# Optimization experiments

Measured on AMD Instinct MI355X. Metric: run time of the kernel, lower is better.

Reference implementation:

```python
import jax, jax.numpy as jnp
import numpy as np

B, N, S, D1, D2 = 16, 4096, 1024, 128, 256
MLP = [256, 128]
BN_EPS = 1e-5


def setup_inputs() -> dict:
    key = jax.random.key(0)
    ks = jax.random.split(key, 12)
    inp = {
        "xyz1": jax.random.normal(ks[0], (B, 3, N), dtype=jnp.float32),
        "xyz2": jax.random.normal(ks[1], (B, 3, S), dtype=jnp.float32),
        "points1": jax.random.normal(ks[2], (B, D1, N), dtype=jnp.float32),
        "points2": jax.random.normal(ks[3], (B, D2, S), dtype=jnp.float32),
    }
    in_ch = D1 + D2  # 384
    chans = [in_ch] + MLP
    ki = 4
    for li in range(len(MLP)):
        cin, cout = chans[li], chans[li + 1]
        inp[f"w{li+1}"] = jax.random.normal(ks[ki], (cout, cin), dtype=jnp.float32) * (1.0 / np.sqrt(cin)); ki += 1
        inp[f"b{li+1}"] = jnp.zeros((cout,), dtype=jnp.float32)
        inp[f"g{li+1}"] = jnp.ones((cout,), dtype=jnp.float32)
        inp[f"beta{li+1}"] = jnp.zeros((cout,), dtype=jnp.float32)
    return inp


def _batchnorm1d(x, gamma, beta):
    # x: [B, C, N]; training-mode batch stats over (B, N)
    mean = jnp.mean(x, axis=(0, 2), keepdims=True)
    var = jnp.var(x, axis=(0, 2), keepdims=True)
    xhat = (x - mean) * jax.lax.rsqrt(var + BN_EPS)
    return xhat * gamma[None, :, None] + beta[None, :, None]


def reference(xyz1, xyz2, points1, points2, w1, b1, g1, beta1, w2, b2, g2, beta2):
    x1 = jnp.transpose(xyz1, (0, 2, 1))   # [B, N, 3]
    x2 = jnp.transpose(xyz2, (0, 2, 1))   # [B, S, 3]
    p2 = jnp.transpose(points2, (0, 2, 1))  # [B, S, D2]

    # squared pairwise distances [B, N, S]
    dists = jnp.sum((x1[:, :, None, :] - x2[:, None, :, :]) ** 2, axis=-1)
    # 3 smallest distances (original sorts then slices top-3)
    neg_d3, idx = jax.lax.top_k(-dists, 3)  # [B, N, 3]
    d3 = -neg_d3
    dist_recip = 1.0 / (d3 + 1e-8)
    weight = dist_recip / jnp.sum(dist_recip, axis=2, keepdims=True)  # [B, N, 3]

    # gather neighbor features: [B, N, 3, D2]
    feats = p2[jnp.arange(p2.shape[0])[:, None, None], idx]
    interp = jnp.sum(feats * weight[..., None], axis=2)  # [B, N, D2]

    p1 = jnp.transpose(points1, (0, 2, 1))  # [B, N, D1]
    new_points = jnp.concatenate([p1, interp], axis=-1)  # [B, N, D1+D2]
    x = jnp.transpose(new_points, (0, 2, 1))  # [B, C, N]

    for w, b, g, bt in ((w1, b1, g1, beta1), (w2, b2, g2, beta2)):
        x = jnp.einsum("oc,bcn->bon", w, x) + b[None, :, None]
        x = _batchnorm1d(x, g, bt)
        x = jax.nn.relu(x)
    return x
```

## Files before the change

### kernel.cpp

```cpp
#include <hip/hip_runtime.h>

typedef unsigned short u16;
typedef unsigned int   u32;
typedef __attribute__((ext_vector_type(8))) short bf16x8;
typedef __attribute__((ext_vector_type(8))) unsigned short u16x8;
typedef __attribute__((ext_vector_type(4))) float f32x4;

#define NB   16
#define NPTS 4096
#define SPTS 1024
#define BNT  65536

#define G2L(src, dst) __builtin_amdgcn_global_load_lds( \
    (const __attribute__((address_space(1))) void*)(src), \
    (__attribute__((address_space(3))) void*)(dst), 16, 0, 0)

__device__ __forceinline__ float bf2f(u16 u){ return __uint_as_float(((u32)u)<<16); }
__device__ __forceinline__ u16 f2bf(float f){
  u32 u = __float_as_uint(f);
  return (u16)((u + 0x7FFFu + ((u>>16)&1u))>>16);
}

__global__ __launch_bounds__(256) void convw_k(const float* __restrict__ w1, const float* __restrict__ w2,
                                               u16* __restrict__ w1b, u16* __restrict__ w2b){
  int i = blockIdx.x*256 + threadIdx.x;
  if (i < 98304) w1b[i] = f2bf(w1[i]);
  else { int j = i - 98304; w2b[j] = f2bf(w2[j]); }
}

__global__ __launch_bounds__(256) void transpose_k(const float* __restrict__ in, u16* __restrict__ out,
                                                   int C, int S, int ostride){
  __shared__ float tl[64][65];
  int t = threadIdx.x;
  int b = blockIdx.y;
  int s0 = blockIdx.x * 64;
  for (int ct = 0; ct < C; ct += 64){
    __syncthreads();
    for (int i = t; i < 4096; i += 256){
      int sl = i & 63, cl = i >> 6;
      tl[sl][cl] = in[((size_t)b*C + ct + cl)*S + s0 + sl];
    }
    __syncthreads();
    for (int i = t; i < 4096; i += 256){
      int cl = i & 63, sl = i >> 6;
      out[((size_t)b*S + s0 + sl)*ostride + ct + cl] = f2bf(tl[sl][cl]);
    }
  }
}

__global__ __launch_bounds__(512) void knn_k(const float* __restrict__ xyz1, const float* __restrict__ xyz2,
                                             const u16* __restrict__ p2t, u16* __restrict__ X){
  __shared__ float4 sxyz[SPTS];
  __shared__ float  pd[8][3][64];
  __shared__ int    pi[8][3][64];
  __shared__ float  swts[3][64];
  __shared__ int    sidx[3][64];
  int t  = threadIdx.x;
  int b  = blockIdx.x >> 6;
  int n0 = (blockIdx.x & 63) << 6;
  const float* x2b = xyz2 + (size_t)b*3*SPTS;
  for (int s = t; s < SPTS; s += 512)
    sxyz[s] = make_float4(x2b[s], x2b[SPTS+s], x2b[2*SPTS+s], 0.f);
  int q = t & 63, g = t >> 6;
  const float* x1b = xyz1 + (size_t)b*3*NPTS;
  int n = n0 + q;
  float qx = x1b[n], qy = x1b[NPTS+n], qz = x1b[2*NPTS+n];
  __syncthreads();

  float d0=3.4e38f, d1=3.4e38f, d2=3.4e38f;
  int   i0=0, i1=0, i2=0;
  int sBeg = g << 7, sEnd = sBeg + 128;
  for (int s = sBeg; s < sEnd; ++s){
    float4 p = sxyz[s];
    float dist;
    {
      #pragma clang fp contract(off)
      float dx = qx - p.x, dy = qy - p.y, dz = qz - p.z;
      dist = ((dx*dx) + (dy*dy)) + (dz*dz);
    }
    if (dist < d2){
      bool c1 = dist < d1, c0 = dist < d0;
      d2 = c1 ? d1 : dist;                 i2 = c1 ? i1 : s;
      float nd1 = c1 ? (c0 ? d0 : dist) : d1;
      int   ni1 = c1 ? (c0 ? i0 : s)    : i1;
      d0 = c0 ? dist : d0;                 i0 = c0 ? s : i0;
      d1 = nd1;                            i1 = ni1;
    }
  }
  pd[g][0][q]=d0; pd[g][1][q]=d1; pd[g][2][q]=d2;
  pi[g][0][q]=i0; pi[g][1][q]=i1; pi[g][2][q]=i2;
  __syncthreads();

  if (t < 64){
    float m0=3.4e38f, m1=3.4e38f, m2=3.4e38f;
    int   j0=0, j1=0, j2=0;
    #pragma unroll
    for (int gg = 0; gg < 8; ++gg){
      #pragma unroll
      for (int p = 0; p < 3; ++p){
        float dist = pd[gg][p][t]; int s = pi[gg][p][t];
        if (dist < m2){
          bool c1 = dist < m1, c0 = dist < m0;
          m2 = c1 ? m1 : dist;                 j2 = c1 ? j1 : s;
          float nd1 = c1 ? (c0 ? m0 : dist) : m1;
          int   ni1 = c1 ? (c0 ? j0 : s)    : j1;
          m0 = c0 ? dist : m0;                 j0 = c0 ? s : j0;
          m1 = nd1;                            j1 = ni1;
        }
      }
    }
    float r0 = 1.f/(m0 + 1e-8f), r1 = 1.f/(m1 + 1e-8f), r2 = 1.f/(m2 + 1e-8f);
    float rs = (r0 + r1) + r2;
    swts[0][t] = r0/rs; swts[1][t] = r1/rs; swts[2][t] = r2/rs;
    sidx[0][t] = j0;    sidx[1][t] = j1;    sidx[2][t] = j2;
  }
  __syncthreads();

  int w = t >> 6, lane = t & 63;
  for (int qq = w*8; qq < w*8 + 8; ++qq){
    float wa = swts[0][qq], wb = swts[1][qq], wc = swts[2][qq];
    int   j0 = sidx[0][qq], j1 = sidx[1][qq], j2 = sidx[2][qq];
    const ushort4 u0 = *(const ushort4*)(p2t + (((size_t)b*SPTS + j0)<<8) + (lane<<2));
    const ushort4 u1 = *(const ushort4*)(p2t + (((size_t)b*SPTS + j1)<<8) + (lane<<2));
    const ushort4 u2 = *(const ushort4*)(p2t + (((size_t)b*SPTS + j2)<<8) + (lane<<2));
    ushort4 ov;
    ov.x = f2bf(wa*bf2f(u0.x) + wb*bf2f(u1.x) + wc*bf2f(u2.x));
    ov.y = f2bf(wa*bf2f(u0.y) + wb*bf2f(u1.y) + wc*bf2f(u2.y));
    ov.z = f2bf(wa*bf2f(u0.z) + wb*bf2f(u1.z) + wc*bf2f(u2.z));
    ov.w = f2bf(wa*bf2f(u0.w) + wb*bf2f(u1.w) + wc*bf2f(u2.w));
    *(ushort4*)(X + ((size_t)b*NPTS + n0 + qq)*384 + 128 + (lane<<2)) = ov;
  }
}

__global__ __launch_bounds__(256) void gemm1_k(const u16* __restrict__ A, const u16* __restrict__ Bw,
                                               u16* __restrict__ Cc,
                                               float* __restrict__ psum, float* __restrict__ psq){
  __shared__ u16 lA[128*64];
  __shared__ u16 lB[256*64];
  float* sums = (float*)lA;
  float* sqs  = sums + 256;
  int t = threadIdx.x, lane = t & 63, wid = t >> 6;
  int rowBase = blockIdx.x << 7;
  int wm = wid >> 1, wn = wid & 1;

  const char* pA[4]; int dAo[4];
  #pragma unroll
  for (int j = 0; j < 4; ++j){
    int L = j*4096 + t*16;
    int row = L >> 7, kb = L & 127;
    int kbs = kb ^ ((row & 7) << 4);
    pA[j] = (const char*)A + (size_t)(rowBase + row)*768 + kbs;
    dAo[j] = j*4096 + wid*1024;
  }
  const char* pB[8]; int dBo[8];
  #pragma unroll
  for (int j = 0; j < 8; ++j){
    int L = j*4096 + t*16;
    int row = L >> 7, kb = L & 127;
    int kbs = kb ^ ((row & 7) << 4);
    pB[j] = (const char*)Bw + (size_t)row*768 + kbs;
    dBo[j] = j*4096 + wid*1024;
  }

  f32x4 z = {0.f,0.f,0.f,0.f};
  f32x4 acc[4][8];
  #pragma unroll
  for (int m = 0; m < 4; ++m)
    #pragma unroll
    for (int n = 0; n < 8; ++n) acc[m][n] = z;

  #pragma unroll
  for (int kt = 0; kt < 6; ++kt){
    size_t ko = (size_t)kt * 128;
    #pragma unroll
    for (int j = 0; j < 4; ++j) G2L(pA[j] + ko, (char*)lA + dAo[j]);
    #pragma unroll
    for (int j = 0; j < 8; ++j) G2L(pB[j] + ko, (char*)lB + dBo[j]);
    __syncthreads();
    #pragma unroll
    for (int ks = 0; ks < 2; ++ks){
      bf16x8 af[4];
      #pragma unroll
      for (int m = 0; m < 4; ++m){
        int row = wm*64 + m*16 + (lane & 15);
        int sw = (row & 7) << 4;
        int kb = (ks*64 + ((lane >> 4) << 4)) ^ sw;
        af[m] = *(const bf16x8*)((const char*)lA + row*128 + kb);
      }
      #pragma unroll
      for (int n = 0; n < 8; ++n){
        int row = wn*128 + n*16 + (lane & 15);
        int sw = (row & 7) << 4;
        int kb = (ks*64 + ((lane >> 4) << 4)) ^ sw;
        bf16x8 bv = *(const bf16x8*)((const char*)lB + row*128 + kb);
        #pragma unroll
        for (int m = 0; m < 4; ++m)
          acc[m][n] = __builtin_amdgcn_mfma_f32_16x16x32_bf16(af[m], bv, acc[m][n], 0, 0, 0);
      }
    }
    __syncthreads();
  }

  sums[t] = 0.f; sqs[t] = 0.f;
  __syncthreads();
  int colb = wn*128 + (lane & 15);
  #pragma unroll
  for (int n = 0; n < 8; ++n){
    float s = 0.f, q = 0.f;
    #pragma unroll
    for (int m = 0; m < 4; ++m){
      #pragma unroll
      for (int r = 0; r < 4; ++r){
        float v = acc[m][n][r];
        s += v; q += v*v;
      }
    }
    s += __shfl_xor(s, 16); s += __shfl_xor(s, 32);
    q += __shfl_xor(q, 16); q += __shfl_xor(q, 32);
    if (lane < 16){
      atomicAdd(&sums[colb + n*16], s);
      atomicAdd(&sqs [colb + n*16], q);
    }
  }
  __syncthreads();
  psum[(size_t)blockIdx.x*256 + t] = sums[t];
  psq [(size_t)blockIdx.x*256 + t] = sqs[t];

  u16* bb = lB;
  int rl0 = ((lane >> 4) << 2);
  #pragma unroll
  for (int h = 0; h < 2; ++h){
    __syncthreads();
    if (wm == h){
      #pragma unroll
      for (int m = 0; m < 4; ++m)
        #pragma unroll
        for (int n = 0; n < 8; ++n)
          #pragma unroll
          for (int r = 0; r < 4; ++r)
            bb[(m*16 + rl0 + r)*256 + colb + n*16] = f2bf(acc[m][n][r]);
    }
    __syncthreads();
    u16* dst = Cc + (size_t)(rowBase + h*64)*256;
    #pragma unroll
    for (int i = 0; i < 8; ++i)
      *(u16x8*)(dst + i*2048 + t*8) = *(const u16x8*)(bb + i*2048 + t*8);
  }
}

__global__ __launch_bounds__(256) void gemm2_k(const u16* __restrict__ A, const u16* __restrict__ Bw,
                                               u16* __restrict__ Cc,
                                               const float* __restrict__ sc, const float* __restrict__ sh,
                                               float* __restrict__ psum, float* __restrict__ psq){
  const int K = 256;
  __shared__ u16 L[16384];
  __shared__ float sums[128], sqs[128];
  int t = threadIdx.x, lane = t & 63, wid = t >> 6;
  int rowBase = blockIdx.x << 7;
  int wm = wid >> 1, wn = wid & 1;

  const char* pB[4]; int dBo[4];
  #pragma unroll
  for (int j = 0; j < 4; ++j){
    int Lo = j*4096 + t*16;
    int row = Lo >> 7, kb = Lo & 127;
    int kbs = kb ^ ((row & 7) << 4);
    pB[j] = (const char*)Bw + ((size_t)row*K)*2 + kbs;
    dBo[j] = 16384 + j*4096 + wid*1024;
  }
  int arow = t & 127, h = t >> 7;
  const u16* pArow = A + (size_t)(rowBase + arow)*K + h*32;
  int asw = (arow & 7) << 4;
  int wAo0 = arow*128 + ((h*64      ) ^ asw);
  int wAo1 = arow*128 + ((h*64 + 16 ) ^ asw);
  int wAo2 = arow*128 + ((h*64 + 32 ) ^ asw);
  int wAo3 = arow*128 + ((h*64 + 48 ) ^ asw);

  f32x4 z = {0.f,0.f,0.f,0.f};
  f32x4 acc[4][4];
  #pragma unroll
  for (int m = 0; m < 4; ++m)
    #pragma unroll
    for (int n = 0; n < 4; ++n) acc[m][n] = z;

  for (int kk = 0; kk < K; kk += 64){
    size_t ko = (size_t)kk * 2;
    #pragma unroll
    for (int j = 0; j < 4; ++j) G2L(pB[j] + ko, (char*)L + dBo[j]);
    u16x8 y0 = *(const u16x8*)(pArow + kk);
    u16x8 y1 = *(const u16x8*)(pArow + kk + 8);
    u16x8 y2 = *(const u16x8*)(pArow + kk + 16);
    u16x8 y3 = *(const u16x8*)(pArow + kk + 24);
    int k0 = kk + h*32;
    bf16x8 o0, o1, o2, o3;
    #pragma unroll
    for (int j = 0; j < 8; ++j){
      float v = bf2f((u16)y0[j]) * sc[k0 + j] + sh[k0 + j];
      o0[j] = (short)f2bf(fmaxf(v, 0.f));
    }
    #pragma unroll
    for (int j = 0; j < 8; ++j){
      float v = bf2f((u16)y1[j]) * sc[k0 + 8 + j] + sh[k0 + 8 + j];
      o1[j] = (short)f2bf(fmaxf(v, 0.f));
    }
    #pragma unroll
    for (int j = 0; j < 8; ++j){
      float v = bf2f((u16)y2[j]) * sc[k0 + 16 + j] + sh[k0 + 16 + j];
      o2[j] = (short)f2bf(fmaxf(v, 0.f));
    }
    #pragma unroll
    for (int j = 0; j < 8; ++j){
      float v = bf2f((u16)y3[j]) * sc[k0 + 24 + j] + sh[k0 + 24 + j];
      o3[j] = (short)f2bf(fmaxf(v, 0.f));
    }
    *(bf16x8*)((char*)L + wAo0) = o0;
    *(bf16x8*)((char*)L + wAo1) = o1;
    *(bf16x8*)((char*)L + wAo2) = o2;
    *(bf16x8*)((char*)L + wAo3) = o3;
    __syncthreads();
    #pragma unroll
    for (int ks = 0; ks < 2; ++ks){
      bf16x8 af[4];
      #pragma unroll
      for (int m = 0; m < 4; ++m){
        int row = wm*64 + m*16 + (lane & 15);
        int sw = (row & 7) << 4;
        int kb = (ks*64 + ((lane >> 4) << 4)) ^ sw;
        af[m] = *(const bf16x8*)((const char*)L + row*128 + kb);
      }
      #pragma unroll
      for (int n = 0; n < 4; ++n){
        int row = wn*64 + n*16 + (lane & 15);
        int sw = (row & 7) << 4;
        int kb = (ks*64 + ((lane >> 4) << 4)) ^ sw;
        bf16x8 bv = *(const bf16x8*)((const char*)L + 16384 + row*128 + kb);
        #pragma unroll
        for (int m = 0; m < 4; ++m)
          acc[m][n] = __builtin_amdgcn_mfma_f32_16x16x32_bf16(af[m], bv, acc[m][n], 0, 0, 0);
      }
    }
    __syncthreads();
  }

  if (t < 128){ sums[t] = 0.f; sqs[t] = 0.f; }
  __syncthreads();
  int colb = wn*64 + (lane & 15);
  int rl0 = ((lane >> 4) << 2);
  #pragma unroll
  for (int n = 0; n < 4; ++n){
    float s = 0.f, q = 0.f;
    #pragma unroll
    for (int m = 0; m < 4; ++m){
      #pragma unroll
      for (int r = 0; r < 4; ++r){
        float v = acc[m][n][r];
        L[(wm*64 + m*16 + rl0 + r)*128 + colb + n*16] = f2bf(v);
        s += v; q += v*v;
      }
    }
    s += __shfl_xor(s, 16); s += __shfl_xor(s, 32);
    q += __shfl_xor(q, 16); q += __shfl_xor(q, 32);
    if (lane < 16){
      atomicAdd(&sums[colb + n*16], s);
      atomicAdd(&sqs [colb + n*16], q);
    }
  }
  __syncthreads();
  if (t < 128){
    psum[(size_t)blockIdx.x*128 + t] = sums[t];
    psq [(size_t)blockIdx.x*128 + t] = sqs[t];
  }
  u16* dst = Cc + (size_t)rowBase*128;
  #pragma unroll
  for (int i = 0; i < 8; ++i)
    *(u16x8*)(dst + i*2048 + t*8) = *(const u16x8*)(L + i*2048 + t*8);
}

__global__ __launch_bounds__(256) void finalize2_k(const float* __restrict__ psum, const float* __restrict__ psq,
                                                   const float* __restrict__ g, const float* __restrict__ bet,
                                                   float* __restrict__ sc, float* __restrict__ sh,
                                                   int C, int NBLK){
  __shared__ float ls[256][8], lq[256][8];
  int c0 = blockIdx.x*8, t = threadIdx.x;
  float s[8], q[8];
  #pragma unroll
  for (int j = 0; j < 8; ++j){ s[j] = 0.f; q[j] = 0.f; }
  for (int rb = t; rb < NBLK; rb += 256){
    const float* ps = psum + (size_t)rb*C + c0;
    const float* pq = psq  + (size_t)rb*C + c0;
    #pragma unroll
    for (int j = 0; j < 8; ++j){ s[j] += ps[j]; q[j] += pq[j]; }
  }
  #pragma unroll
  for (int j = 0; j < 8; ++j){ ls[t][j] = s[j]; lq[t][j] = q[j]; }
  __syncthreads();
  for (int off = 128; off; off >>= 1){
    if (t < off){
      #pragma unroll
      for (int j = 0; j < 8; ++j){ ls[t][j] += ls[t+off][j]; lq[t][j] += lq[t+off][j]; }
    }
    __syncthreads();
  }
  if (t < 8){
    int c = c0 + t;
    const float inv = 1.f/65536.f;
    float mean = ls[0][t]*inv;
    float var  = lq[0][t]*inv - mean*mean;
    float rstd = rsqrtf(var + 1e-5f);
    float scl  = g[c]*rstd;
    sc[c] = scl;
    sh[c] = bet[c] - mean*scl;
  }
}

__global__ __launch_bounds__(256) void finalout_k(const u16* __restrict__ y2, const float* __restrict__ sc,
                                                  const float* __restrict__ sh, float* __restrict__ out){
  __shared__ float tl[128][65];
  int t  = threadIdx.x;
  int b  = blockIdx.x >> 6;
  int n0 = (blockIdx.x & 63) << 6;
  for (int i = t; i < 8192; i += 256){
    int r = i >> 7, c = i & 127;
    float v = bf2f(y2[((size_t)b*NPTS + n0 + r)*128 + c]);
    v = fmaxf(v*sc[c] + sh[c], 0.f);
    tl[c][r] = v;
  }
  __syncthreads();
  for (int i = t; i < 8192; i += 256){
    int o = i >> 6, j = i & 63;
    out[(size_t)b*128*NPTS + (size_t)o*NPTS + n0 + j] = tl[o][j];
  }
}

extern "C" void kernel_launch(void* const* d_in, const int* in_sizes, int n_in,
                              void* d_out, int out_size, void* d_ws, size_t ws_size,
                              hipStream_t stream) {
  const float* xyz1    = (const float*)d_in[0];
  const float* xyz2    = (const float*)d_in[1];
  const float* points1 = (const float*)d_in[2];
  const float* points2 = (const float*)d_in[3];
  const float* w1      = (const float*)d_in[4];
  const float* g1      = (const float*)d_in[6];
  const float* beta1   = (const float*)d_in[7];
  const float* w2      = (const float*)d_in[8];
  const float* g2      = (const float*)d_in[10];
  const float* beta2   = (const float*)d_in[11];

  char* ws = (char*)d_ws;
  u16*  X    = (u16*)ws;
  u16*  Y2   = (u16*)ws;
  u16*  Y1   = (u16*)(ws + 50331648);
  u16*  p2t  = (u16*)(ws + 83886080);
  u16*  w1b  = (u16*)(ws + 92274688);
  u16*  w2b  = (u16*)(ws + 92471296);
  float* psum1 = (float*)(ws + 83886080);
  float* psq1  = (float*)(ws + 84934656);
  float* psum2 = (float*)(ws + 85983232);
  float* psq2  = (float*)(ws + 86507520);
  float* sc1   = (float*)(ws + 87031808);
  float* sh1   = (float*)(ws + 87032832);
  float* sc2   = (float*)(ws + 87033856);
  float* sh2   = (float*)(ws + 87034368);

  convw_k<<<512, 256, 0, stream>>>(w1, w2, w1b, w2b);
  transpose_k<<<dim3(64, 16), 256, 0, stream>>>(points1, X,   128, NPTS, 384);
  transpose_k<<<dim3(16, 16), 256, 0, stream>>>(points2, p2t, 256, SPTS, 256);
  knn_k<<<1024, 512, 0, stream>>>(xyz1, xyz2, p2t, X);
  gemm1_k<<<512, 256, 0, stream>>>(X, w1b, Y1, psum1, psq1);
  finalize2_k<<<32, 256, 0, stream>>>(psum1, psq1, g1, beta1, sc1, sh1, 256, 512);
  gemm2_k<<<512, 256, 0, stream>>>(Y1, w2b, Y2, sc1, sh1, psum2, psq2);
  finalize2_k<<<16, 256, 0, stream>>>(psum2, psq2, g2, beta2, sc2, sh2, 128, 512);
  finalout_k<<<1024, 256, 0, stream>>>(Y2, sc2, sh2, (float*)d_out);
}
```

Before: 144.4 us.

## Double-buffer LDS K-tiles in both GEMM kernels to overlap loads with MFMA

Both GEMM kernels now split K into 32-wide tiles held in two LDS buffers. The next tile's global-to-LDS loads (and in gemm2, the BN+ReLU transform of the A tile) are issued while MFMAs run on the current buffer, with one barrier per step. The swizzle is adapted to the 64-byte row pitch. This is meant to hide global load latency behind compute, at the cost of twice as many loop iterations and barriers and extra register pressure for the prefetched A values.

```diff
diff --git a/kernel.cpp b/kernel.cpp
--- a/kernel.cpp
+++ b/kernel.cpp
@@ -135,29 +135,29 @@
 __global__ __launch_bounds__(256) void gemm1_k(const u16* __restrict__ A, const u16* __restrict__ Bw,
                                                u16* __restrict__ Cc,
                                                float* __restrict__ psum, float* __restrict__ psq){
-  __shared__ u16 lA[128*64];
-  __shared__ u16 lB[256*64];
+  __shared__ u16 lA[2][128*32];
+  __shared__ u16 lB[2][256*32];
   float* sums = (float*)lA;
   float* sqs  = sums + 256;
   int t = threadIdx.x, lane = t & 63, wid = t >> 6;
   int rowBase = blockIdx.x << 7;
   int wm = wid >> 1, wn = wid & 1;
 
-  const char* pA[4]; int dAo[4];
+  const char* pA[2]; int dAo[2];
+  #pragma unroll
+  for (int j = 0; j < 2; ++j){
+    int L = j*4096 + t*16;
+    int row = L >> 6, kb = L & 63;
+    int kbs = kb ^ (((row >> 1) & 3) << 4);
+    pA[j] = (const char*)A + (size_t)(rowBase + row)*768 + kbs;
+    dAo[j] = j*4096 + wid*1024;
+  }
+  const char* pB[4]; int dBo[4];
   #pragma unroll
   for (int j = 0; j < 4; ++j){
     int L = j*4096 + t*16;
-    int row = L >> 7, kb = L & 127;
-    int kbs = kb ^ ((row & 7) << 4);
-    pA[j] = (const char*)A + (size_t)(rowBase + row)*768 + kbs;
-    dAo[j] = j*4096 + wid*1024;
-  }
-  const char* pB[8]; int dBo[8];
-  #pragma unroll
-  for (int j = 0; j < 8; ++j){
-    int L = j*4096 + t*16;
-    int row = L >> 7, kb = L & 127;
-    int kbs = kb ^ ((row & 7) << 4);
+    int row = L >> 6, kb = L & 63;
+    int kbs = kb ^ (((row >> 1) & 3) << 4);
     pB[j] = (const char*)Bw + (size_t)row*768 + kbs;
     dBo[j] = j*4096 + wid*1024;
   }
@@ -170,33 +170,36 @@
     for (int n = 0; n < 8; ++n) acc[m][n] = z;
 
   #pragma unroll
-  for (int kt = 0; kt < 6; ++kt){
-    size_t ko = (size_t)kt * 128;
-    #pragma unroll
-    for (int j = 0; j < 4; ++j) G2L(pA[j] + ko, (char*)lA + dAo[j]);
-    #pragma unroll
-    for (int j = 0; j < 8; ++j) G2L(pB[j] + ko, (char*)lB + dBo[j]);
-    __syncthreads();
-    #pragma unroll
-    for (int ks = 0; ks < 2; ++ks){
-      bf16x8 af[4];
-      #pragma unroll
-      for (int m = 0; m < 4; ++m){
-        int row = wm*64 + m*16 + (lane & 15);
-        int sw = (row & 7) << 4;
-        int kb = (ks*64 + ((lane >> 4) << 4)) ^ sw;
-        af[m] = *(const bf16x8*)((const char*)lA + row*128 + kb);
-      }
-      #pragma unroll
-      for (int n = 0; n < 8; ++n){
-        int row = wn*128 + n*16 + (lane & 15);
-        int sw = (row & 7) << 4;
-        int kb = (ks*64 + ((lane >> 4) << 4)) ^ sw;
-        bf16x8 bv = *(const bf16x8*)((const char*)lB + row*128 + kb);
-        #pragma unroll
-        for (int m = 0; m < 4; ++m)
-          acc[m][n] = __builtin_amdgcn_mfma_f32_16x16x32_bf16(af[m], bv, acc[m][n], 0, 0, 0);
-      }
+  for (int j = 0; j < 2; ++j) G2L(pA[j], (char*)lA[0] + dAo[j]);
+  #pragma unroll
+  for (int j = 0; j < 4; ++j) G2L(pB[j], (char*)lB[0] + dBo[j]);
+  __syncthreads();
+
+  #pragma unroll
+  for (int kt = 0; kt < 12; ++kt){
+    const int cur = kt & 1;
+    if (kt < 11){
+      size_t ko = (size_t)(kt + 1) * 64;
+      #pragma unroll
+      for (int j = 0; j < 2; ++j) G2L(pA[j] + ko, (char*)lA[cur^1] + dAo[j]);
+      #pragma unroll
+      for (int j = 0; j < 4; ++j) G2L(pB[j] + ko, (char*)lB[cur^1] + dBo[j]);
+    }
+    bf16x8 af[4];
+    #pragma unroll
+    for (int m = 0; m < 4; ++m){
+      int row = wm*64 + m*16 + (lane & 15);
+      int kb = ((lane >> 4) << 4) ^ (((row >> 1) & 3) << 4);
+      af[m] = *(const bf16x8*)((const char*)lA[cur] + row*64 + kb);
+    }
+    #pragma unroll
+    for (int n = 0; n < 8; ++n){
+      int row = wn*128 + n*16 + (lane & 15);
+      int kb = ((lane >> 4) << 4) ^ (((row >> 1) & 3) << 4);
+      bf16x8 bv = *(const bf16x8*)((const char*)lB[cur] + row*64 + kb);
+      #pragma unroll
+      for (int m = 0; m < 4; ++m)
+        acc[m][n] = __builtin_amdgcn_mfma_f32_16x16x32_bf16(af[m], bv, acc[m][n], 0, 0, 0);
     }
     __syncthreads();
   }
@@ -226,7 +229,7 @@
   psum[(size_t)blockIdx.x*256 + t] = sums[t];
   psq [(size_t)blockIdx.x*256 + t] = sqs[t];
 
-  u16* bb = lB;
+  u16* bb = (u16*)lB;
   int rl0 = ((lane >> 4) << 2);
   #pragma unroll
   for (int h = 0; h < 2; ++h){
@@ -259,22 +262,20 @@
   int rowBase = blockIdx.x << 7;
   int wm = wid >> 1, wn = wid & 1;
 
-  const char* pB[4]; int dBo[4];
-  #pragma unroll
-  for (int j = 0; j < 4; ++j){
+  const char* pB[2]; int dBo[2];
+  #pragma unroll
+  for (int j = 0; j < 2; ++j){
     int Lo = j*4096 + t*16;
-    int row = Lo >> 7, kb = Lo & 127;
-    int kbs = kb ^ ((row & 7) << 4);
+    int row = Lo >> 6, kb = Lo & 63;
+    int kbs = kb ^ (((row >> 1) & 3) << 4);
     pB[j] = (const char*)Bw + ((size_t)row*K)*2 + kbs;
-    dBo[j] = 16384 + j*4096 + wid*1024;
+    dBo[j] = j*4096 + wid*1024;
   }
   int arow = t & 127, h = t >> 7;
-  const u16* pArow = A + (size_t)(rowBase + arow)*K + h*32;
-  int asw = (arow & 7) << 4;
-  int wAo0 = arow*128 + ((h*64      ) ^ asw);
-  int wAo1 = arow*128 + ((h*64 + 16 ) ^ asw);
-  int wAo2 = arow*128 + ((h*64 + 32 ) ^ asw);
-  int wAo3 = arow*128 + ((h*64 + 48 ) ^ asw);
+  const u16* pArow = A + (size_t)(rowBase + arow)*K + h*16;
+  int asw = ((arow >> 1) & 3) << 4;
+  int wAo0 = arow*64 + ((h*32      ) ^ asw);
+  int wAo1 = arow*64 + ((h*32 + 16 ) ^ asw);
 
   f32x4 z = {0.f,0.f,0.f,0.f};
   f32x4 acc[4][4];
@@ -283,16 +284,13 @@
     #pragma unroll
     for (int n = 0; n < 4; ++n) acc[m][n] = z;
 
-  for (int kk = 0; kk < K; kk += 64){
-    size_t ko = (size_t)kk * 2;
-    #pragma unroll
-    for (int j = 0; j < 4; ++j) G2L(pB[j] + ko, (char*)L + dBo[j]);
-    u16x8 y0 = *(const u16x8*)(pArow + kk);
-    u16x8 y1 = *(const u16x8*)(pArow + kk + 8);
-    u16x8 y2 = *(const u16x8*)(pArow + kk + 16);
-    u16x8 y3 = *(const u16x8*)(pArow + kk + 24);
-    int k0 = kk + h*32;
-    bf16x8 o0, o1, o2, o3;
+  {
+    u16x8 y0 = *(const u16x8*)(pArow);
+    u16x8 y1 = *(const u16x8*)(pArow + 8);
+    #pragma unroll
+    for (int j = 0; j < 2; ++j) G2L(pB[j], (char*)L + 16384 + dBo[j]);
+    int k0 = h*16;
+    bf16x8 o0, o1;
     #pragma unroll
     for (int j = 0; j < 8; ++j){
       float v = bf2f((u16)y0[j]) * sc[k0 + j] + sh[k0 + j];
@@ -303,41 +301,53 @@
       float v = bf2f((u16)y1[j]) * sc[k0 + 8 + j] + sh[k0 + 8 + j];
       o1[j] = (short)f2bf(fmaxf(v, 0.f));
     }
-    #pragma unroll
-    for (int j = 0; j < 8; ++j){
-      float v = bf2f((u16)y2[j]) * sc[k0 + 16 + j] + sh[k0 + 16 + j];
-      o2[j] = (short)f2bf(fmaxf(v, 0.f));
-    }
-    #pragma unroll
-    for (int j = 0; j < 8; ++j){
-      float v = bf2f((u16)y3[j]) * sc[k0 + 24 + j] + sh[k0 + 24 + j];
-      o3[j] = (short)f2bf(fmaxf(v, 0.f));
-    }
     *(bf16x8*)((char*)L + wAo0) = o0;
     *(bf16x8*)((char*)L + wAo1) = o1;
-    *(bf16x8*)((char*)L + wAo2) = o2;
-    *(bf16x8*)((char*)L + wAo3) = o3;
-    __syncthreads();
-    #pragma unroll
-    for (int ks = 0; ks < 2; ++ks){
-      bf16x8 af[4];
-      #pragma unroll
-      for (int m = 0; m < 4; ++m){
-        int row = wm*64 + m*16 + (lane & 15);
-        int sw = (row & 7) << 4;
-        int kb = (ks*64 + ((lane >> 4) << 4)) ^ sw;
-        af[m] = *(const bf16x8*)((const char*)L + row*128 + kb);
+  }
+  __syncthreads();
+
+  #pragma unroll
+  for (int kt = 0; kt < 8; ++kt){
+    const int cur = kt & 1;
+    u16x8 ny0 = {}, ny1 = {};
+    if (kt < 7){
+      ny0 = *(const u16x8*)(pArow + (kt+1)*32);
+      ny1 = *(const u16x8*)(pArow + (kt+1)*32 + 8);
+      size_t ko = (size_t)(kt + 1) * 64;
+      #pragma unroll
+      for (int j = 0; j < 2; ++j) G2L(pB[j] + ko, (char*)L + 16384 + (cur^1)*8192 + dBo[j]);
+    }
+    bf16x8 af[4];
+    #pragma unroll
+    for (int m = 0; m < 4; ++m){
+      int row = wm*64 + m*16 + (lane & 15);
+      int kb = ((lane >> 4) << 4) ^ (((row >> 1) & 3) << 4);
+      af[m] = *(const bf16x8*)((const char*)L + cur*8192 + row*64 + kb);
+    }
+    #pragma unroll
+    for (int n = 0; n < 4; ++n){
+      int row = wn*64 + n*16 + (lane & 15);
+      int kb = ((lane >> 4) << 4) ^ (((row >> 1) & 3) << 4);
+      bf16x8 bv = *(const bf16x8*)((const char*)L + 16384 + cur*8192 + row*64 + kb);
+      #pragma unroll
+      for (int m = 0; m < 4; ++m)
+        acc[m][n] = __builtin_amdgcn_mfma_f32_16x16x32_bf16(af[m], bv, acc[m][n], 0, 0, 0);
+    }
+    if (kt < 7){
+      int k0 = (kt+1)*32 + h*16;
+      bf16x8 o0, o1;
+      #pragma unroll
+      for (int j = 0; j < 8; ++j){
+        float v = bf2f((u16)ny0[j]) * sc[k0 + j] + sh[k0 + j];
+        o0[j] = (short)f2bf(fmaxf(v, 0.f));
       }
       #pragma unroll
-      for (int n = 0; n < 4; ++n){
-        int row = wn*64 + n*16 + (lane & 15);
-        int sw = (row & 7) << 4;
-        int kb = (ks*64 + ((lane >> 4) << 4)) ^ sw;
-        bf16x8 bv = *(const bf16x8*)((const char*)L + 16384 + row*128 + kb);
-        #pragma unroll
-        for (int m = 0; m < 4; ++m)
-          acc[m][n] = __builtin_amdgcn_mfma_f32_16x16x32_bf16(af[m], bv, acc[m][n], 0, 0, 0);
+      for (int j = 0; j < 8; ++j){
+        float v = bf2f((u16)ny1[j]) * sc[k0 + 8 + j] + sh[k0 + 8 + j];
+        o1[j] = (short)f2bf(fmaxf(v, 0.f));
       }
+      *(bf16x8*)((char*)L + (cur^1)*8192 + wAo0) = o0;
+      *(bf16x8*)((char*)L + (cur^1)*8192 + wAo1) = o1;
     }
     __syncthreads();
   }
```

After: 148.2 us. +2.6%, slower.
